# Kernel optimization log

Measured on AMD Instinct MI355X. Metric: run time of the kernel, lower is better.

## Reference

```python
import jax, jax.numpy as jnp
import numpy as np

T, B, N, D, H = 128, 64, 24, 256, 8
F = D // H  # 32


def setup_inputs() -> dict:
    key = jax.random.key(0)
    ks = jax.random.split(key, 7)
    s = 1.0 / np.sqrt(D)  # torch nn.Linear default init range
    inputs = jax.random.normal(ks[0], (T, B, N * D), dtype=jnp.float32)
    Wk = jax.random.uniform(ks[1], (H, F, D), minval=-s, maxval=s, dtype=jnp.float32)
    bk = jax.random.uniform(ks[2], (H, F), minval=-s, maxval=s, dtype=jnp.float32)
    Wv = jax.random.uniform(ks[3], (H, F, D), minval=-s, maxval=s, dtype=jnp.float32)
    bv = jax.random.uniform(ks[4], (H, F), minval=-s, maxval=s, dtype=jnp.float32)
    Wq = jax.random.uniform(ks[5], (H, N, F, D), minval=-s, maxval=s, dtype=jnp.float32)
    bq = jax.random.uniform(ks[6], (H, N, F), minval=-s, maxval=s, dtype=jnp.float32)
    return {"inputs": inputs, "Wk": Wk, "bk": bk, "Wv": Wv, "bv": bv, "Wq": Wq, "bq": bq}


def reference(inputs, Wk, bk, Wv, bv, Wq, bq):
    # inputs: (T, B, N*D) -> (T, B, N, D)
    x = inputs.reshape(T, B, N, D)
    # shared K/V per head: (T, B, H, N, F)
    k = jnp.einsum('tbnd,hfd->tbhnf', x, Wk) + bk[:, None, :]
    v = jnp.einsum('tbnd,hfd->tbhnf', x, Wv) + bv[:, None, :]
    # per-joint Q: joint n uses its own (F, D) weight -> (T, B, H, N, F)
    q = jnp.einsum('tbnd,hnfd->tbhnf', x, Wq) + bq
    # attention over joints, scaled by sqrt(F)
    scores = jnp.einsum('tbhnf,tbhmf->tbhnm', q, k) / jnp.sqrt(jnp.float32(F))
    attn = jax.nn.softmax(scores, axis=-1)
    out = jnp.einsum('tbhnm,tbhmf->tbhnf', attn, v)
    # concat heads along feature dim per joint, then flatten joints: (T, B, N*H*F)
    out = out.transpose(0, 1, 3, 2, 4).reshape(T, B, N * H * F)
    # dropout is identity in eval mode
    return out
```

## Files before the change

### kernel.cpp

```cpp
#include <hip/hip_runtime.h>
#include <hip/hip_bf16.h>
#include <cstdio>

#define TB  8192
#define N_  24
#define D_  256
#define H_  8
#define F_  32
#define ND  6144
#define HNF 6144

typedef unsigned short u16;
typedef __attribute__((ext_vector_type(8))) _Float16 f16x8;
typedef __attribute__((ext_vector_type(8))) short bf16x8;
typedef __attribute__((ext_vector_type(4))) float f32x4;

__device__ __forceinline__ u16 f2b(float f) {
    unsigned int u = __float_as_uint(f);
    return (u16)((u + 0x7FFFu + ((u >> 16) & 1u)) >> 16);
}
__device__ __forceinline__ float b2f(u16 s) {
    return __uint_as_float(((unsigned int)s) << 16);
}
__device__ __forceinline__ u16 f2h(float f) {
    _Float16 h = (_Float16)f;
    u16 u; __builtin_memcpy(&u, &h, 2); return u;
}

__device__ __forceinline__ void gl_lds16(const void* g, void* l) {
    __builtin_amdgcn_global_load_lds(
        (const __attribute__((address_space(1))) unsigned int*)g,
        (__attribute__((address_space(3))) unsigned int*)l, 16, 0, 0);
}

__global__ __launch_bounds__(256) void prep_all(
    const float* __restrict__ Wk, const float* __restrict__ Wv,
    const float* __restrict__ Wq,
    const float* __restrict__ bk, const float* __restrict__ bv,
    const float* __restrict__ bq,
    u16* __restrict__ Bp, float* __restrict__ biasp)
{
    const int idx = blockIdx.x * 256 + threadIdx.x;
    if (idx < 24 * 8 * 48 * 64) {
        const int fr = idx & 15;
        const int fq = (idx >> 4) & 3;
        const int g  = (idx >> 6) % 48;
        const int kt = (idx / (64 * 48)) % 8;
        const int n  = idx / (64 * 48 * 8);
        const int col = g * 16 + fr;
        const int d0  = kt * 32 + fq * 8;
        const int c   = col & 255;
        const float* src;
        if (col < 256)      src = Wk + (size_t)c * 256 + d0;
        else if (col < 512) src = Wv + (size_t)c * 256 + d0;
        else {
            const int h = c >> 5, f = c & 31;
            src = Wq + ((size_t)(h * 24 + n) * 32 + f) * 256 + d0;
        }
        __align__(16) u16 out[8];
        #pragma unroll
        for (int j = 0; j < 8; ++j) out[j] = f2h(src[j]);
        *reinterpret_cast<uint4*>(Bp + (size_t)idx * 8) =
            *reinterpret_cast<const uint4*>(out);
    } else if (idx < 24 * 8 * 48 * 64 + 24 * 768) {
        const int bi  = idx - 24 * 8 * 48 * 64;
        const int col = bi % 768, n = bi / 768;
        const int c = col & 255;
        float v;
        if (col < 256)      v = bk[c];
        else if (col < 512) v = bv[c];
        else { const int h = c >> 5, f = c & 31; v = bq[(h * 24 + n) * 32 + f]; }
        biasp[n * 768 + col] = v;
    }
}

__global__ __launch_bounds__(512, 4) void proj_mfma(
    const float* __restrict__ x,
    const u16* __restrict__ Bp,
    const float* __restrict__ biasp,
    u16* __restrict__ kb, u16* __restrict__ vb, u16* __restrict__ qb)
{
    const int b    = blockIdx.x;
    const int xcd  = b & 7;
    const int t    = b >> 3;
    const int gi   = t % 9;
    const int mblk = t / 9;
    const int grp  = xcd * 9 + gi;
    const int n    = grp / 3;
    const int ct   = grp % 3;
    const int tb0  = mblk * 128;
    const int tid  = threadIdx.x;
    const int w    = tid >> 6;
    const int lane = tid & 63;
    const int wm   = w >> 2;
    const int wn   = w & 3;
    const int fr   = lane & 15, fq = lane >> 4;

    __shared__ __align__(16) char smem[81920];
    char* const Ab = smem;
    char* const Bb = smem + 49152;

    const int arow8 = lane >> 3;
    const int clog  = (lane & 7) ^ arow8;
    const char* asrc = (const char*)x +
        (size_t)(tb0 + w * 16 + arow8) * (ND * 4) + n * 1024 + clog * 16;

    const size_t bbase = (size_t)(n * 8 * 48 + ct * 16 + w * 2) * 1024 + lane * 16;

    f32x4 acc[4][4];
    #pragma unroll
    for (int m = 0; m < 4; ++m)
        #pragma unroll
        for (int j = 0; j < 4; ++j) acc[m][j] = (f32x4){0.f, 0.f, 0.f, 0.f};

    #pragma unroll
    for (int q = 0; q < 2; ++q)
        gl_lds16(asrc + q * (8 * ND * 4), Ab + (w * 2 + q) * 1024);
    gl_lds16((const char*)Bp + bbase,        Bb + (w * 2) * 1024);
    gl_lds16((const char*)Bp + bbase + 1024, Bb + (w * 2 + 1) * 1024);
    #pragma unroll
    for (int q = 0; q < 2; ++q)
        gl_lds16(asrc + q * (8 * ND * 4) + 128, Ab + 16384 + (w * 2 + q) * 1024);
    asm volatile("s_waitcnt vmcnt(2)" ::: "memory");
    __builtin_amdgcn_s_barrier();
    asm volatile("" ::: "memory");

    #pragma unroll
    for (int kt = 0; kt < 8; ++kt) {
        const int ab  = kt % 3;
        const int bbf = kt & 1;

        if (kt < 7) {
            const size_t bs = bbase + (size_t)(kt + 1) * 49152;
            gl_lds16((const char*)Bp + bs,        Bb + (bbf ^ 1) * 16384 + (w * 2) * 1024);
            gl_lds16((const char*)Bp + bs + 1024, Bb + (bbf ^ 1) * 16384 + (w * 2 + 1) * 1024);
        }
        if (kt < 6) {
            #pragma unroll
            for (int q = 0; q < 2; ++q)
                gl_lds16(asrc + q * (8 * ND * 4) + (kt + 2) * 128,
                         Ab + ((kt + 2) % 3) * 16384 + (w * 2 + q) * 1024);
        }

        f16x8 bfr[4], afr[4];
        #pragma unroll
        for (int j = 0; j < 4; ++j)
            bfr[j] = *reinterpret_cast<const f16x8*>(
                Bb + bbf * 16384 + (wn * 4 + j) * 1024 + lane * 16);
        #pragma unroll
        for (int m = 0; m < 4; ++m) {
            const int row = wm * 64 + m * 16 + fr;
            const int c0  = (2 * fq) ^ (fr & 7);
            const f32x4 lo = *reinterpret_cast<const f32x4*>(
                Ab + ab * 16384 + row * 128 + c0 * 16);
            const f32x4 hi = *reinterpret_cast<const f32x4*>(
                Ab + ab * 16384 + row * 128 + (c0 ^ 1) * 16);
            f16x8 af;
            #pragma unroll
            for (int e = 0; e < 4; ++e) {
                af[e]     = (_Float16)lo[e];
                af[4 + e] = (_Float16)hi[e];
            }
            afr[m] = af;
        }

        __builtin_amdgcn_s_setprio(1);
        #pragma unroll
        for (int j = 0; j < 4; ++j)
            #pragma unroll
            for (int m = 0; m < 4; ++m)
                acc[m][j] = __builtin_amdgcn_mfma_f32_16x16x32_f16(
                    afr[m], bfr[j], acc[m][j], 0, 0, 0);
        __builtin_amdgcn_s_setprio(0);

        if (kt < 7) {
            if (kt < 6) { asm volatile("s_waitcnt vmcnt(2)" ::: "memory"); }
            else        { asm volatile("s_waitcnt vmcnt(0)" ::: "memory"); }
            __builtin_amdgcn_s_barrier();
            asm volatile("" ::: "memory");
        }
    }
    __syncthreads();

    u16* dst = (ct == 0) ? kb : (ct == 1) ? vb : qb;
    #pragma unroll
    for (int p = 0; p < 2; ++p) {
        if (wm == p) {
            #pragma unroll
            for (int j = 0; j < 4; ++j) {
                const int colL = wn * 64 + j * 16 + fr;
                const float bs = biasp[n * 768 + ct * 256 + colL];
                #pragma unroll
                for (int m = 0; m < 4; ++m)
                    #pragma unroll
                    for (int r = 0; r < 4; ++r) {
                        const int rowL = m * 16 + fq * 4 + r;
                        const int byte = (rowL * 512 + colL * 2) ^ ((rowL & 7) << 4);
                        *reinterpret_cast<u16*>(smem + byte) = f2b(acc[m][j][r] + bs);
                    }
            }
        }
        __syncthreads();
        #pragma unroll
        for (int it = 0; it < 4; ++it) {
            const int id  = it * 512 + tid;
            const int row = id >> 5;
            const int cch = id & 31;
            const uint4 v = *reinterpret_cast<const uint4*>(
                smem + ((row * 512 + cch * 16) ^ ((row & 7) << 4)));
            *reinterpret_cast<uint4*>(
                &dst[(size_t)(tb0 + p * 64 + row) * HNF + n * 256 + cch * 8]) = v;
        }
        __syncthreads();
    }
}

__device__ __forceinline__ int swz(int row, int chunk) {
    return row * 32 + (((chunk ^ ((row >> 1) ^ (row >> 3))) & 3) << 3);
}

__global__ __launch_bounds__(256) void attn_mfma(
    const u16* __restrict__ kb,
    const u16* __restrict__ vb,
    const u16* __restrict__ qb,
    float* __restrict__ out)
{
    const int tid  = threadIdx.x;
    const int wid  = tid >> 6;
    const int lane = tid & 63;
    const int fr   = lane & 15;
    const int fq   = lane >> 4;
    const size_t tb = (size_t)blockIdx.x * 4 + wid;

    __shared__ __align__(16) u16 lds[4][2048];
    u16* Pw = lds[wid];
    u16* Vt = lds[wid] + 1024;

    #pragma unroll
    for (int i = 0; i < 4; ++i)
        reinterpret_cast<uint4*>(lds[wid])[lane + i * 64] = (uint4){0, 0, 0, 0};

    const u16* qt = qb + tb * HNF;
    const u16* kt = kb + tb * HNF;
    const u16* vt = vb + tb * HNF;
    float* outp = out + tb * ND;

    const float scale = 0.17677669529663687f;
    const bool colok = fr < 8;

    for (int h = 0; h < H_; ++h) {
        const u16* qh = qt + h * 32;
        const u16* kh = kt + h * 32;
        const u16* vh = vt + h * 32;

        bf16x8 qa[2], ka[2];
        #pragma unroll
        for (int t = 0; t < 2; ++t) {
            int rq = t * 16 + fr; rq = rq < 24 ? rq : 23;
            qa[t] = *reinterpret_cast<const bf16x8*>(qh + rq * 256 + fq * 8);
            ka[t] = *reinterpret_cast<const bf16x8*>(kh + rq * 256 + fq * 8);
        }

        {
            const int m = lane >> 2, q = lane & 3;
            const uint4 vv = *reinterpret_cast<const uint4*>(vh + m * 256 + q * 8);
            #pragma unroll
            for (int j = 0; j < 8; ++j) {
                const int f = q * 8 + j;
                Vt[swz(f, m >> 3) + (m & 7)] = reinterpret_cast<const u16*>(&vv)[j];
            }
            if (lane < 32) {
                const int m2 = 16 + (lane >> 2), q2 = lane & 3;
                const uint4 v2 = *reinterpret_cast<const uint4*>(vh + m2 * 256 + q2 * 8);
                #pragma unroll
                for (int j = 0; j < 8; ++j) {
                    const int f = q2 * 8 + j;
                    Vt[swz(f, m2 >> 3) + (m2 & 7)] = reinterpret_cast<const u16*>(&v2)[j];
                }
            }
        }

        f32x4 S[2][2];
        #pragma unroll
        for (int a = 0; a < 2; ++a)
            #pragma unroll
            for (int bb = 0; bb < 2; ++bb)
                S[a][bb] = __builtin_amdgcn_mfma_f32_16x16x32_bf16(
                    qa[a], ka[bb], (f32x4){0.f, 0.f, 0.f, 0.f}, 0, 0, 0);

        float inv[2][4];
        #pragma unroll
        for (int t = 0; t < 2; ++t) {
            float e0[4], e1[4];
            #pragma unroll
            for (int r = 0; r < 4; ++r) {
                const float a = S[t][0][r] * scale;
                const float bbv = colok ? S[t][1][r] * scale : -1e30f;
                float mx = fmaxf(a, bbv);
                #pragma unroll
                for (int off = 1; off < 16; off <<= 1)
                    mx = fmaxf(mx, __shfl_xor(mx, off));
                e0[r] = __expf(a - mx);
                e1[r] = colok ? __expf(bbv - mx) : 0.f;
                float sm = e0[r] + e1[r];
                #pragma unroll
                for (int off = 1; off < 16; off <<= 1)
                    sm += __shfl_xor(sm, off);
                inv[t][r] = 1.f / sm;
            }
            #pragma unroll
            for (int r = 0; r < 4; ++r) {
                const int row = t * 16 + fq * 4 + r;
                if (row < 24) {
                    Pw[swz(row, fr >> 3) + (fr & 7)] = f2b(e0[r]);
                    if (colok) {
                        const int c1 = 16 + fr;
                        Pw[swz(row, c1 >> 3) + (c1 & 7)] = f2b(e1[r]);
                    }
                }
            }
        }

        bf16x8 pa[2], vbf[2];
        #pragma unroll
        for (int t = 0; t < 2; ++t)
            pa[t] = *reinterpret_cast<const bf16x8*>(&Pw[swz(t * 16 + fr, fq)]);
        #pragma unroll
        for (int t = 0; t < 2; ++t)
            vbf[t] = *reinterpret_cast<const bf16x8*>(&Vt[swz(t * 16 + fr, fq)]);

        f32x4 O[2][2];
        #pragma unroll
        for (int a = 0; a < 2; ++a)
            #pragma unroll
            for (int bb = 0; bb < 2; ++bb)
                O[a][bb] = __builtin_amdgcn_mfma_f32_16x16x32_bf16(
                    pa[a], vbf[bb], (f32x4){0.f, 0.f, 0.f, 0.f}, 0, 0, 0);

        #pragma unroll
        for (int a = 0; a < 2; ++a)
            #pragma unroll
            for (int r = 0; r < 4; ++r) {
                const int row = a * 16 + fq * 4 + r;
                if (row < 24) {
                    outp[row * D_ + h * F_ + fr]      = O[a][0][r] * inv[a][r];
                    outp[row * D_ + h * F_ + 16 + fr] = O[a][1][r] * inv[a][r];
                }
            }
    }
}

extern "C" void kernel_launch(void* const* d_in, const int* in_sizes, int n_in,
                              void* d_out, int out_size, void* d_ws, size_t ws_size,
                              hipStream_t stream) {
    const float* x  = (const float*)d_in[0];
    const float* Wk = (const float*)d_in[1];
    const float* bk = (const float*)d_in[2];
    const float* Wv = (const float*)d_in[3];
    const float* bv = (const float*)d_in[4];
    const float* Wq = (const float*)d_in[5];
    const float* bq = (const float*)d_in[6];
    float* out = (float*)d_out;

    const size_t qkv_elems = (size_t)TB * HNF;
    const size_t need = qkv_elems * 2ull * 3ull;
    if (ws_size < need) fprintf(stderr, "ws too small: %zu < %zu\n", ws_size, need);
    u16* kbuf = (u16*)d_ws;
    u16* vbuf = kbuf + qkv_elems;
    u16* qbuf = vbuf + qkv_elems;

    u16*   Bp    = (u16*)d_out;
    float* biasp = (float*)((char*)d_out + (size_t)24 * 8 * 48 * 512 * 2);

    prep_all<<<2376, 256, 0, stream>>>(Wk, Wv, Wq, bk, bv, bq, Bp, biasp);
    proj_mfma<<<4608, 512, 0, stream>>>(x, Bp, biasp, kbuf, vbuf, qbuf);
    attn_mfma<<<TB / 4, 256, 0, stream>>>(kbuf, vbuf, qbuf, out);
}
```

Measured before the change: 286.4 us.

## Replace LDS-staged projection GEMM with register-direct loads and smaller tiles

The projection kernel stops staging A and B tiles through LDS with global_load_lds and barriers. Each wave now loads its fp32 activations and fp16 weight fragments straight into registers, double-buffered across k-steps. The block tile shrinks from 128x256 to 64x128 with 256 threads, which quadruples the grid and drops all barriers from the main loop. In exchange, each wave fetches activations without sharing through LDS, so global and L2 traffic rise and per-wave data reuse falls.

```diff
diff --git a/kernel.cpp b/kernel.cpp
--- a/kernel.cpp
+++ b/kernel.cpp
@@ -25,12 +25,6 @@
 __device__ __forceinline__ u16 f2h(float f) {
     _Float16 h = (_Float16)f;
     u16 u; __builtin_memcpy(&u, &h, 2); return u;
-}
-
-__device__ __forceinline__ void gl_lds16(const void* g, void* l) {
-    __builtin_amdgcn_global_load_lds(
-        (const __attribute__((address_space(1))) unsigned int*)g,
-        (__attribute__((address_space(3))) unsigned int*)l, 16, 0, 0);
 }
 
 __global__ __launch_bounds__(256) void prep_all(
@@ -74,7 +68,7 @@
     }
 }
 
-__global__ __launch_bounds__(512, 4) void proj_mfma(
+__global__ __launch_bounds__(256, 3) void proj_mfma(
     const float* __restrict__ x,
     const u16* __restrict__ Bp,
     const float* __restrict__ biasp,
@@ -83,135 +77,109 @@
     const int b    = blockIdx.x;
     const int xcd  = b & 7;
     const int t    = b >> 3;
-    const int gi   = t % 9;
-    const int mblk = t / 9;
-    const int grp  = xcd * 9 + gi;
-    const int n    = grp / 3;
-    const int ct   = grp % 3;
-    const int tb0  = mblk * 128;
+    const int pi   = t % 18;
+    const int mblk = t / 18;
+    const int grp  = xcd * 18 + pi;
+    const int n    = grp / 6;
+    const int colt = grp % 6;
     const int tid  = threadIdx.x;
     const int w    = tid >> 6;
     const int lane = tid & 63;
-    const int wm   = w >> 2;
-    const int wn   = w & 3;
+    const int wm   = w >> 1;
+    const int wn   = w & 1;
     const int fr   = lane & 15, fq = lane >> 4;
 
-    __shared__ __align__(16) char smem[81920];
-    char* const Ab = smem;
-    char* const Bb = smem + 49152;
-
-    const int arow8 = lane >> 3;
-    const int clog  = (lane & 7) ^ arow8;
-    const char* asrc = (const char*)x +
-        (size_t)(tb0 + w * 16 + arow8) * (ND * 4) + n * 1024 + clog * 16;
-
-    const size_t bbase = (size_t)(n * 8 * 48 + ct * 16 + w * 2) * 1024 + lane * 16;
-
-    f32x4 acc[4][4];
-    #pragma unroll
-    for (int m = 0; m < 4; ++m)
+    __shared__ __align__(16) u16 tile[64][128];
+
+    const float* a0 = x + (size_t)(mblk * 64 + wm * 32 + fr) * ND + n * 256 + fq * 8;
+    const float* a1 = a0 + (size_t)16 * ND;
+    const u16* bb = Bp + ((size_t)(n * 8) * 48 + colt * 8 + wn * 4) * 512 + lane * 8;
+
+    f32x4 acc[2][4];
+    #pragma unroll
+    for (int m = 0; m < 2; ++m)
         #pragma unroll
         for (int j = 0; j < 4; ++j) acc[m][j] = (f32x4){0.f, 0.f, 0.f, 0.f};
 
-    #pragma unroll
-    for (int q = 0; q < 2; ++q)
-        gl_lds16(asrc + q * (8 * ND * 4), Ab + (w * 2 + q) * 1024);
-    gl_lds16((const char*)Bp + bbase,        Bb + (w * 2) * 1024);
-    gl_lds16((const char*)Bp + bbase + 1024, Bb + (w * 2 + 1) * 1024);
-    #pragma unroll
-    for (int q = 0; q < 2; ++q)
-        gl_lds16(asrc + q * (8 * ND * 4) + 128, Ab + 16384 + (w * 2 + q) * 1024);
-    asm volatile("s_waitcnt vmcnt(2)" ::: "memory");
-    __builtin_amdgcn_s_barrier();
-    asm volatile("" ::: "memory");
+    float4 aR[2][4];
+    f16x8  bR[2][4];
+
+    aR[0][0] = *reinterpret_cast<const float4*>(a0);
+    aR[0][1] = *reinterpret_cast<const float4*>(a0 + 4);
+    aR[0][2] = *reinterpret_cast<const float4*>(a1);
+    aR[0][3] = *reinterpret_cast<const float4*>(a1 + 4);
+    #pragma unroll
+    for (int j = 0; j < 4; ++j)
+        bR[0][j] = *reinterpret_cast<const f16x8*>(bb + j * 512);
 
     #pragma unroll
     for (int kt = 0; kt < 8; ++kt) {
-        const int ab  = kt % 3;
-        const int bbf = kt & 1;
+        const int c = kt & 1, o = c ^ 1;
 
         if (kt < 7) {
-            const size_t bs = bbase + (size_t)(kt + 1) * 49152;
-            gl_lds16((const char*)Bp + bs,        Bb + (bbf ^ 1) * 16384 + (w * 2) * 1024);
-            gl_lds16((const char*)Bp + bs + 1024, Bb + (bbf ^ 1) * 16384 + (w * 2 + 1) * 1024);
-        }
-        if (kt < 6) {
-            #pragma unroll
-            for (int q = 0; q < 2; ++q)
-                gl_lds16(asrc + q * (8 * ND * 4) + (kt + 2) * 128,
-                         Ab + ((kt + 2) % 3) * 16384 + (w * 2 + q) * 1024);
-        }
-
-        f16x8 bfr[4], afr[4];
+            const float* an0 = a0 + (kt + 1) * 32;
+            const float* an1 = a1 + (kt + 1) * 32;
+            aR[o][0] = *reinterpret_cast<const float4*>(an0);
+            aR[o][1] = *reinterpret_cast<const float4*>(an0 + 4);
+            aR[o][2] = *reinterpret_cast<const float4*>(an1);
+            aR[o][3] = *reinterpret_cast<const float4*>(an1 + 4);
+            const u16* bn = bb + (size_t)(kt + 1) * 24576;
+            #pragma unroll
+            for (int j = 0; j < 4; ++j)
+                bR[o][j] = *reinterpret_cast<const f16x8*>(bn + j * 512);
+        }
+
+        f16x8 af[2];
+        #pragma unroll
+        for (int m = 0; m < 2; ++m) {
+            #pragma unroll
+            for (int e = 0; e < 4; ++e) {
+                af[m][e]     = (_Float16)aR[c][m * 2][e];
+                af[m][4 + e] = (_Float16)aR[c][m * 2 + 1][e];
+            }
+        }
+
+        __builtin_amdgcn_s_setprio(1);
         #pragma unroll
         for (int j = 0; j < 4; ++j)
-            bfr[j] = *reinterpret_cast<const f16x8*>(
-                Bb + bbf * 16384 + (wn * 4 + j) * 1024 + lane * 16);
-        #pragma unroll
-        for (int m = 0; m < 4; ++m) {
-            const int row = wm * 64 + m * 16 + fr;
-            const int c0  = (2 * fq) ^ (fr & 7);
-            const f32x4 lo = *reinterpret_cast<const f32x4*>(
-                Ab + ab * 16384 + row * 128 + c0 * 16);
-            const f32x4 hi = *reinterpret_cast<const f32x4*>(
-                Ab + ab * 16384 + row * 128 + (c0 ^ 1) * 16);
-            f16x8 af;
-            #pragma unroll
-            for (int e = 0; e < 4; ++e) {
-                af[e]     = (_Float16)lo[e];
-                af[4 + e] = (_Float16)hi[e];
-            }
-            afr[m] = af;
-        }
-
-        __builtin_amdgcn_s_setprio(1);
-        #pragma unroll
-        for (int j = 0; j < 4; ++j)
-            #pragma unroll
-            for (int m = 0; m < 4; ++m)
+            #pragma unroll
+            for (int m = 0; m < 2; ++m)
                 acc[m][j] = __builtin_amdgcn_mfma_f32_16x16x32_f16(
-                    afr[m], bfr[j], acc[m][j], 0, 0, 0);
+                    af[m], bR[c][j], acc[m][j], 0, 0, 0);
         __builtin_amdgcn_s_setprio(0);
-
-        if (kt < 7) {
-            if (kt < 6) { asm volatile("s_waitcnt vmcnt(2)" ::: "memory"); }
-            else        { asm volatile("s_waitcnt vmcnt(0)" ::: "memory"); }
-            __builtin_amdgcn_s_barrier();
-            asm volatile("" ::: "memory");
-        }
+    }
+
+    float bv4[4];
+    #pragma unroll
+    for (int j = 0; j < 4; ++j)
+        bv4[j] = biasp[n * 768 + colt * 128 + wn * 64 + j * 16 + fr];
+
+    #pragma unroll
+    for (int j = 0; j < 4; ++j) {
+        const int colL = wn * 64 + j * 16 + fr;
+        #pragma unroll
+        for (int m = 0; m < 2; ++m)
+            #pragma unroll
+            for (int r = 0; r < 4; ++r) {
+                const int row = wm * 32 + m * 16 + fq * 4 + r;
+                const int byte = row * 256 + ((colL * 2) ^ ((row & 7) << 4));
+                *reinterpret_cast<u16*>((char*)tile + byte) = f2b(acc[m][j][r] + bv4[j]);
+            }
     }
     __syncthreads();
 
+    const int ct = colt >> 1;
     u16* dst = (ct == 0) ? kb : (ct == 1) ? vb : qb;
-    #pragma unroll
-    for (int p = 0; p < 2; ++p) {
-        if (wm == p) {
-            #pragma unroll
-            for (int j = 0; j < 4; ++j) {
-                const int colL = wn * 64 + j * 16 + fr;
-                const float bs = biasp[n * 768 + ct * 256 + colL];
-                #pragma unroll
-                for (int m = 0; m < 4; ++m)
-                    #pragma unroll
-                    for (int r = 0; r < 4; ++r) {
-                        const int rowL = m * 16 + fq * 4 + r;
-                        const int byte = (rowL * 512 + colL * 2) ^ ((rowL & 7) << 4);
-                        *reinterpret_cast<u16*>(smem + byte) = f2b(acc[m][j][r] + bs);
-                    }
-            }
-        }
-        __syncthreads();
-        #pragma unroll
-        for (int it = 0; it < 4; ++it) {
-            const int id  = it * 512 + tid;
-            const int row = id >> 5;
-            const int cch = id & 31;
-            const uint4 v = *reinterpret_cast<const uint4*>(
-                smem + ((row * 512 + cch * 16) ^ ((row & 7) << 4)));
-            *reinterpret_cast<uint4*>(
-                &dst[(size_t)(tb0 + p * 64 + row) * HNF + n * 256 + cch * 8]) = v;
-        }
-        __syncthreads();
+    const int colb = (colt & 1) * 128;
+    #pragma unroll
+    for (int it = 0; it < 4; ++it) {
+        const int id  = it * 256 + tid;
+        const int row = id >> 4;
+        const int cch = id & 15;
+        const uint4 v = *reinterpret_cast<const uint4*>(
+            (char*)tile + row * 256 + ((cch * 16) ^ ((row & 7) << 4)));
+        *reinterpret_cast<uint4*>(
+            &dst[(size_t)(mblk * 64 + row) * HNF + n * 256 + colb + cch * 8]) = v;
     }
 }
 
@@ -373,6 +341,6 @@
     float* biasp = (float*)((char*)d_out + (size_t)24 * 8 * 48 * 512 * 2);
 
     prep_all<<<2376, 256, 0, stream>>>(Wk, Wv, Wq, bk, bv, bq, Bp, biasp);
-    proj_mfma<<<4608, 512, 0, stream>>>(x, Bp, biasp, kbuf, vbuf, qbuf);
+    proj_mfma<<<18432, 256, 0, stream>>>(x, Bp, biasp, kbuf, vbuf, qbuf);
     attn_mfma<<<TB / 4, 256, 0, stream>>>(kbuf, vbuf, qbuf, out);
 }
```

Measured after the change: 508.9 us. 1.78x slower.
